# Optimization experiments

Hardware: AMD Instinct MI355X
Metric: run time of the kernel (lower is better)

The kernel has to match this reference:

```python
import jax, jax.numpy as jnp
import numpy as np

B, C, H, W_ = 4, 256, 64, 64
INTER = 128

def conv1x1(x, w, b):
    # x: [B,C,H,W], w: [O,C], b: [O] -> [B,O,H,W]
    return jnp.einsum('bchw,oc->bohw', x, w) + b[None, :, None, None]

def setup_inputs() -> dict:
    key = jax.random.key(0)
    ks = jax.random.split(key, 5)
    s_in = 1.0 / np.sqrt(C)
    s_mid = 1.0 / np.sqrt(INTER)
    return {
        'x': jax.random.normal(ks[0], (B, C, H, W_), dtype=jnp.float32),
        'w_g': jax.random.normal(ks[1], (INTER, C), dtype=jnp.float32) * s_in,
        'b_g': jnp.zeros((INTER,), dtype=jnp.float32),
        'w_theta': jax.random.normal(ks[2], (INTER, C), dtype=jnp.float32) * s_in,
        'b_theta': jnp.zeros((INTER,), dtype=jnp.float32),
        'w_phi': jax.random.normal(ks[3], (INTER, C), dtype=jnp.float32) * s_in,
        'b_phi': jnp.zeros((INTER,), dtype=jnp.float32),
        'w_out': jax.random.normal(ks[4], (C, INTER), dtype=jnp.float32) * s_mid,
        'b_out': jnp.zeros((C,), dtype=jnp.float32),
    }

def reference(x, w_g, b_g, w_theta, b_theta, w_phi, b_phi, w_out, b_out):
    b, c, h, w = x.shape
    n = h * w
    # 1x1 conv projections, flatten spatial dims to N tokens
    g_x = conv1x1(x, w_g, b_g).reshape(b, INTER, n).transpose(0, 2, 1)      # [B,N,I]
    theta_x = conv1x1(x, w_theta, b_theta).reshape(b, INTER, n).transpose(0, 2, 1)  # [B,N,I]
    phi_x = conv1x1(x, w_phi, b_phi).reshape(b, INTER, n)                   # [B,I,N]
    f = jnp.einsum('bni,bim->bnm', theta_x, phi_x)                          # [B,N,N]
    f_div_C = jax.nn.softmax(f, axis=-1)
    y = jnp.einsum('bnm,bmi->bni', f_div_C, g_x)                            # [B,N,I]
    y = y.transpose(0, 2, 1).reshape(b, INTER, h, w)
    W_y = conv1x1(y, w_out, b_out)                                          # [B,C,H,W]
    return W_y + x
```

## Files before the change

### kernel.cpp

```cpp
#include <hip/hip_runtime.h>

#define BB 4
#define CC 256
#define NN 4096
#define II 128
#define NSPLIT 4
#define KVH (NN / NSPLIT)
#define NT (KVH / 64)
#define LOG2E 1.4426950408889634f

typedef float f32x4 __attribute__((ext_vector_type(4)));
typedef _Float16 f16x8 __attribute__((ext_vector_type(8)));

static __device__ __forceinline__ unsigned short f2h(float f) {
    _Float16 h = (_Float16)f;
    return __builtin_bit_cast(unsigned short, h);
}
static __device__ __forceinline__ float h2f(unsigned short s) {
    return (float)__builtin_bit_cast(_Float16, s);
}
static __device__ __forceinline__ unsigned int pack2h(float a, float b) {
    return (unsigned int)f2h(a) | ((unsigned int)f2h(b) << 16);
}
static __device__ __forceinline__ unsigned int cvt2h(float a, float b) {
    return __builtin_bit_cast(unsigned int, __builtin_amdgcn_cvt_pkrtz(a, b));
}
#define M3(a, b, c) fmaxf(fmaxf((a), (b)), (c))

__global__ __launch_bounds__(256) void proj_kernel(
    const float* __restrict__ x,
    const float* __restrict__ w_th, const float* __restrict__ b_th,
    const float* __restrict__ w_ph, const float* __restrict__ b_ph,
    const float* __restrict__ w_g,  const float* __restrict__ b_g,
    const float* __restrict__ w_out,
    unsigned short* __restrict__ Qb, unsigned short* __restrict__ Kb,
    unsigned short* __restrict__ Vt, unsigned short* __restrict__ Wo)
{
    __shared__ char lds[24576];
    unsigned short* wl = (unsigned short*)lds;
    unsigned short* xl = (unsigned short*)(lds + 16384);

    int tid = threadIdx.x;
    int w = tid >> 6, l = tid & 63, g = l >> 4, cl = l & 15;
    int mat = blockIdx.z, b = blockIdx.y, n0 = blockIdx.x * 64;
    const float* wp = (mat == 0) ? w_th : (mat == 1) ? w_ph : w_g;
    const float* bp = (mat == 0) ? b_th : (mat == 1) ? b_ph : b_g;

    f32x4 acc[2][4];
    #pragma unroll
    for (int it = 0; it < 2; ++it)
        #pragma unroll
        for (int nt = 0; nt < 4; ++nt) acc[it][nt] = (f32x4){0.f, 0.f, 0.f, 0.f};

    const float* xb = x + (size_t)b * CC * NN;
    int c2 = tid >> 3, nch = tid & 7;

    for (int c0 = 0; c0 < CC; c0 += 64) {
        __syncthreads();
        #pragma unroll
        for (int r = 0; r < 4; ++r) {
            int idx = r * 256 + tid;
            int row = idx >> 3, ch = idx & 7;
            const float* src = wp + row * CC + c0 + ch * 8;
            float4 a = *(const float4*)src;
            float4 bq = *(const float4*)(src + 4);
            union { unsigned int u[4]; uint4 q; } pk;
            pk.u[0] = pack2h(a.x, a.y);  pk.u[1] = pack2h(a.z, a.w);
            pk.u[2] = pack2h(bq.x, bq.y); pk.u[3] = pack2h(bq.z, bq.w);
            *(uint4*)((char*)wl + row * 128 + ((ch ^ (row & 7)) << 4)) = pk.q;
        }
        {
            const float* xsrc = xb + (size_t)(c0 + c2 * 2) * NN + n0 + nch * 8;
            float4 x00 = *(const float4*)xsrc;
            float4 x01 = *(const float4*)(xsrc + 4);
            float4 x10 = *(const float4*)(xsrc + NN);
            float4 x11 = *(const float4*)(xsrc + NN + 4);
            float lo[8] = {x00.x, x00.y, x00.z, x00.w, x01.x, x01.y, x01.z, x01.w};
            float hi[8] = {x10.x, x10.y, x10.z, x10.w, x11.x, x11.y, x11.z, x11.w};
            #pragma unroll
            for (int t = 0; t < 8; ++t) {
                int n = nch * 8 + t;
                *(unsigned int*)((char*)xl + n * 128 + ((c2 * 4) ^ ((n & 7) << 4))) = pack2h(lo[t], hi[t]);
            }
        }
        __syncthreads();
        #pragma unroll
        for (int kc = 0; kc < 2; ++kc) {
            f16x8 af[2], bf[4];
            #pragma unroll
            for (int it = 0; it < 2; ++it) {
                int row = w * 32 + it * 16 + cl;
                af[it] = *(const f16x8*)((const char*)wl + row * 128 + (((kc * 4 + g) ^ (row & 7)) << 4));
            }
            #pragma unroll
            for (int nt = 0; nt < 4; ++nt) {
                int row = nt * 16 + cl;
                bf[nt] = *(const f16x8*)((const char*)xl + row * 128 + (((kc * 4 + g) ^ (row & 7)) << 4));
            }
            #pragma unroll
            for (int it = 0; it < 2; ++it)
                #pragma unroll
                for (int nt = 0; nt < 4; ++nt)
                    acc[it][nt] = __builtin_amdgcn_mfma_f32_16x16x32_f16(af[it], bf[nt], acc[it][nt], 0, 0, 0);
        }
    }

    float bv[2][4];
    #pragma unroll
    for (int it = 0; it < 2; ++it)
        #pragma unroll
        for (int r = 0; r < 4; ++r) bv[it][r] = bp[w * 32 + it * 16 + 4 * g + r];
    float scale = (mat == 0) ? LOG2E : 1.0f;

    __syncthreads();
    if (mat < 2) {
        unsigned short* pk = (unsigned short*)lds;
        #pragma unroll
        for (int it = 0; it < 2; ++it)
            #pragma unroll
            for (int nt = 0; nt < 4; ++nt)
                #pragma unroll
                for (int r = 0; r < 4; r += 2) {
                    int n = nt * 16 + cl;
                    int i = w * 32 + it * 16 + 4 * g + r;
                    unsigned int v = pack2h((acc[it][nt][r] + bv[it][r]) * scale,
                                            (acc[it][nt][r + 1] + bv[it][r + 1]) * scale);
                    *(unsigned int*)((char*)pk + n * 256 + ((i * 2) ^ ((n & 7) << 4))) = v;
                }
        __syncthreads();
        unsigned short* out = (mat == 0) ? Qb : Kb;
        #pragma unroll
        for (int r = 0; r < 4; ++r) {
            int idx = r * 256 + tid;
            int n = idx >> 4, seg = idx & 15;
            uint4 q = *(const uint4*)((const char*)pk + n * 256 + ((seg << 4) ^ ((n & 7) << 4)));
            *(uint4*)(out + (size_t)(b * NN + n0 + n) * II + seg * 8) = q;
        }
    } else {
        unsigned short* pk = (unsigned short*)lds;
        #pragma unroll
        for (int it = 0; it < 2; ++it)
            #pragma unroll
            for (int nt = 0; nt < 4; ++nt)
                #pragma unroll
                for (int r = 0; r < 4; ++r) {
                    int i = w * 32 + it * 16 + 4 * g + r;
                    int n = nt * 16 + cl;
                    *(unsigned short*)((char*)pk + i * 128 + ((n * 2) ^ ((i & 7) << 4))) =
                        f2h(acc[it][nt][r] + bv[it][r]);
                }
        __syncthreads();
        #pragma unroll
        for (int r = 0; r < 4; ++r) {
            int idx = r * 256 + tid;
            int i = idx >> 3, seg = idx & 7;
            uint4 q = *(const uint4*)((const char*)pk + i * 128 + ((seg << 4) ^ ((i & 7) << 4)));
            *(uint4*)(Vt + (size_t)(b * II + i) * NN + n0 + seg * 8) = q;
        }
        if (blockIdx.x == 0) {
            #pragma unroll
            for (int r = 0; r < 16; ++r) {
                int idx = (r * 256 + tid) * 8;
                float4 a = *(const float4*)(w_out + idx);
                float4 b4 = *(const float4*)(w_out + idx + 4);
                union { unsigned int u[4]; uint4 q; } pw;
                pw.u[0] = pack2h(a.x, a.y);   pw.u[1] = pack2h(a.z, a.w);
                pw.u[2] = pack2h(b4.x, b4.y); pw.u[3] = pack2h(b4.z, b4.w);
                *(uint4*)&Wo[idx] = pw.q;
            }
        }
    }
}

__global__ __launch_bounds__(256, 2) void attn_kernel(
    const unsigned short* __restrict__ Qb,
    const unsigned short* __restrict__ Kb,
    const unsigned short* __restrict__ Vb,
    unsigned short* __restrict__ Yp,
    float2* __restrict__ ML)
{
    __shared__ unsigned short Ks[64 * 128];
    __shared__ unsigned short Vs[128 * 64];

    int tid = threadIdx.x;
    int w = tid >> 6, l = tid & 63, g = l >> 4, cl = l & 15;
    int id = blockIdx.x;
    int comb = (id & 7) * 2 + ((id >> 3) & 1);
    int b = comb >> 2, sp = comb & 3, qt = id >> 4;
    int qr0 = qt * 128;
    int m_base = sp * KVH;

    f16x8 qa0[4], qa1[4];
    {
        const unsigned short* qrow0 = Qb + (size_t)(b * NN + qr0 + w * 32 + cl) * II;
        const unsigned short* qrow1 = qrow0 + 16 * II;
        #pragma unroll
        for (int kc = 0; kc < 4; ++kc) {
            qa0[kc] = *(const f16x8*)(qrow0 + kc * 32 + g * 8);
            qa1[kc] = *(const f16x8*)(qrow1 + kc * 32 + g * 8);
        }
    }
    const f16x8 onesv = {(_Float16)1.f, (_Float16)1.f, (_Float16)1.f, (_Float16)1.f,
                         (_Float16)1.f, (_Float16)1.f, (_Float16)1.f, (_Float16)1.f};

    f32x4 yacc0[8], yacc1[8], lacc0, lacc1;
    #pragma unroll
    for (int it = 0; it < 8; ++it) {
        yacc0[it] = (f32x4){0.f, 0.f, 0.f, 0.f};
        yacc1[it] = (f32x4){0.f, 0.f, 0.f, 0.f};
    }
    lacc0 = (f32x4){0.f, 0.f, 0.f, 0.f};
    lacc1 = (f32x4){0.f, 0.f, 0.f, 0.f};
    float mrun0 = -1e30f, mrun1 = -1e30f;

    const unsigned short* kb = Kb + (size_t)(b * NN + m_base) * II;
    const unsigned short* vb = Vb + (size_t)b * II * NN + m_base;
    int krow = tid >> 4, kch = tid & 15;
    int vrow = tid >> 3, vch = tid & 7;
    int kswz = (kch ^ (krow & 7)) << 4;
    int vsw = (vrow & 7) << 4;
    int vc0 = ((vch >> 2) * 32 + (vch & 1) * 16 + ((vch >> 1) & 1) * 4) * 2;

    uint4 k0, k1, k2, k3, v0, v1, v2, v3;
    k0 = *(const uint4*)(kb + (size_t)(krow) * II + kch * 8);
    k1 = *(const uint4*)(kb + (size_t)(16 + krow) * II + kch * 8);
    k2 = *(const uint4*)(kb + (size_t)(32 + krow) * II + kch * 8);
    k3 = *(const uint4*)(kb + (size_t)(48 + krow) * II + kch * 8);
    v0 = *(const uint4*)(vb + (size_t)(vrow) * NN + vch * 8);
    v1 = *(const uint4*)(vb + (size_t)(32 + vrow) * NN + vch * 8);
    v2 = *(const uint4*)(vb + (size_t)(64 + vrow) * NN + vch * 8);
    v3 = *(const uint4*)(vb + (size_t)(96 + vrow) * NN + vch * 8);

    for (int t = 0; t < NT; ++t) {
        __syncthreads();
        *(uint4*)((char*)Ks + (krow) * 256 + kswz) = k0;
        *(uint4*)((char*)Ks + (16 + krow) * 256 + kswz) = k1;
        *(uint4*)((char*)Ks + (32 + krow) * 256 + kswz) = k2;
        *(uint4*)((char*)Ks + (48 + krow) * 256 + kswz) = k3;
        {
            uint2 lo, hi;
            lo.x = v0.x; lo.y = v0.y; hi.x = v0.z; hi.y = v0.w;
            *(uint2*)((char*)Vs + (vrow) * 128 + (vc0 ^ vsw)) = lo;
            *(uint2*)((char*)Vs + (vrow) * 128 + ((vc0 + 16) ^ vsw)) = hi;
            lo.x = v1.x; lo.y = v1.y; hi.x = v1.z; hi.y = v1.w;
            *(uint2*)((char*)Vs + (32 + vrow) * 128 + (vc0 ^ vsw)) = lo;
            *(uint2*)((char*)Vs + (32 + vrow) * 128 + ((vc0 + 16) ^ vsw)) = hi;
            lo.x = v2.x; lo.y = v2.y; hi.x = v2.z; hi.y = v2.w;
            *(uint2*)((char*)Vs + (64 + vrow) * 128 + (vc0 ^ vsw)) = lo;
            *(uint2*)((char*)Vs + (64 + vrow) * 128 + ((vc0 + 16) ^ vsw)) = hi;
            lo.x = v3.x; lo.y = v3.y; hi.x = v3.z; hi.y = v3.w;
            *(uint2*)((char*)Vs + (96 + vrow) * 128 + (vc0 ^ vsw)) = lo;
            *(uint2*)((char*)Vs + (96 + vrow) * 128 + ((vc0 + 16) ^ vsw)) = hi;
        }
        __syncthreads();
        if (t + 1 < NT) {
            const unsigned short* kp = kb + (size_t)(t + 1) * 64 * II;
            k0 = *(const uint4*)(kp + (size_t)(krow) * II + kch * 8);
            k1 = *(const uint4*)(kp + (size_t)(16 + krow) * II + kch * 8);
            k2 = *(const uint4*)(kp + (size_t)(32 + krow) * II + kch * 8);
            k3 = *(const uint4*)(kp + (size_t)(48 + krow) * II + kch * 8);
        }

        f32x4 s0[4], s1[4];
        #pragma unroll
        for (int mt = 0; mt < 4; ++mt) {
            s0[mt] = (f32x4){0.f, 0.f, 0.f, 0.f};
            s1[mt] = (f32x4){0.f, 0.f, 0.f, 0.f};
        }
        __builtin_amdgcn_s_setprio(1);
        #pragma unroll
        for (int mt = 0; mt < 4; ++mt) {
            int row = mt * 16 + cl;
            #pragma unroll
            for (int kc = 0; kc < 4; ++kc) {
                f16x8 kf = *(const f16x8*)((const char*)Ks + row * 256 + (((kc * 4 + g) ^ (row & 7)) << 4));
                s0[mt] = __builtin_amdgcn_mfma_f32_16x16x32_f16(kf, qa0[kc], s0[mt], 0, 0, 0);
                s1[mt] = __builtin_amdgcn_mfma_f32_16x16x32_f16(kf, qa1[kc], s1[mt], 0, 0, 0);
            }
        }
        __builtin_amdgcn_s_setprio(0);
        if (t + 1 < NT) {
            const unsigned short* vp = vb + (size_t)(t + 1) * 64;
            v0 = *(const uint4*)(vp + (size_t)(vrow) * NN + vch * 8);
            v1 = *(const uint4*)(vp + (size_t)(32 + vrow) * NN + vch * 8);
            v2 = *(const uint4*)(vp + (size_t)(64 + vrow) * NN + vch * 8);
            v3 = *(const uint4*)(vp + (size_t)(96 + vrow) * NN + vch * 8);
        }

        union { unsigned int u[4]; f16x8 v; } pb00, pb01, pb10, pb11;
        {
            float t0 = M3(s0[0][0], s0[0][1], s0[0][2]);
            float t1 = M3(s0[0][3], s0[1][0], s0[1][1]);
            float t2 = M3(s0[1][2], s0[1][3], s0[2][0]);
            float t3 = M3(s0[2][1], s0[2][2], s0[2][3]);
            float t4 = M3(s0[3][0], s0[3][1], s0[3][2]);
            float tmax = fmaxf(M3(t0, t1, t2), M3(t3, t4, s0[3][3]));
            tmax = fmaxf(tmax, __shfl_xor(tmax, 16));
            tmax = fmaxf(tmax, __shfl_xor(tmax, 32));
            if (!__all(tmax <= mrun0 + 8.0f)) {
                float mnew = fmaxf(mrun0, tmax);
                float corr = exp2f(mrun0 - mnew);
                mrun0 = mnew;
                #pragma unroll
                for (int it = 0; it < 8; ++it)
                    #pragma unroll
                    for (int r = 0; r < 4; ++r) yacc0[it][r] *= corr;
                #pragma unroll
                for (int r = 0; r < 4; ++r) lacc0[r] *= corr;
            }
            #pragma unroll
            for (int mt = 0; mt < 4; ++mt) {
                unsigned int ua = cvt2h(exp2f(s0[mt][0] - mrun0), exp2f(s0[mt][1] - mrun0));
                unsigned int ub = cvt2h(exp2f(s0[mt][2] - mrun0), exp2f(s0[mt][3] - mrun0));
                if (mt < 2) { pb00.u[mt * 2] = ua; pb00.u[mt * 2 + 1] = ub; }
                else        { pb01.u[(mt - 2) * 2] = ua; pb01.u[(mt - 2) * 2 + 1] = ub; }
            }
        }
        {
            float t0 = M3(s1[0][0], s1[0][1], s1[0][2]);
            float t1 = M3(s1[0][3], s1[1][0], s1[1][1]);
            float t2 = M3(s1[1][2], s1[1][3], s1[2][0]);
            float t3 = M3(s1[2][1], s1[2][2], s1[2][3]);
            float t4 = M3(s1[3][0], s1[3][1], s1[3][2]);
            float tmax = fmaxf(M3(t0, t1, t2), M3(t3, t4, s1[3][3]));
            tmax = fmaxf(tmax, __shfl_xor(tmax, 16));
            tmax = fmaxf(tmax, __shfl_xor(tmax, 32));
            if (!__all(tmax <= mrun1 + 8.0f)) {
                float mnew = fmaxf(mrun1, tmax);
                float corr = exp2f(mrun1 - mnew);
                mrun1 = mnew;
                #pragma unroll
                for (int it = 0; it < 8; ++it)
                    #pragma unroll
                    for (int r = 0; r < 4; ++r) yacc1[it][r] *= corr;
                #pragma unroll
                for (int r = 0; r < 4; ++r) lacc1[r] *= corr;
            }
            #pragma unroll
            for (int mt = 0; mt < 4; ++mt) {
                unsigned int ua = cvt2h(exp2f(s1[mt][0] - mrun1), exp2f(s1[mt][1] - mrun1));
                unsigned int ub = cvt2h(exp2f(s1[mt][2] - mrun1), exp2f(s1[mt][3] - mrun1));
                if (mt < 2) { pb10.u[mt * 2] = ua; pb10.u[mt * 2 + 1] = ub; }
                else        { pb11.u[(mt - 2) * 2] = ua; pb11.u[(mt - 2) * 2 + 1] = ub; }
            }
        }

        __builtin_amdgcn_s_setprio(1);
        lacc0 = __builtin_amdgcn_mfma_f32_16x16x32_f16(onesv, pb00.v, lacc0, 0, 0, 0);
        lacc0 = __builtin_amdgcn_mfma_f32_16x16x32_f16(onesv, pb01.v, lacc0, 0, 0, 0);
        lacc1 = __builtin_amdgcn_mfma_f32_16x16x32_f16(onesv, pb10.v, lacc1, 0, 0, 0);
        lacc1 = __builtin_amdgcn_mfma_f32_16x16x32_f16(onesv, pb11.v, lacc1, 0, 0, 0);
        #pragma unroll
        for (int it = 0; it < 8; ++it) {
            int row = it * 16 + cl;
            f16x8 vf0 = *(const f16x8*)((const char*)Vs + row * 128 + ((g ^ (row & 7)) << 4));
            f16x8 vf1 = *(const f16x8*)((const char*)Vs + row * 128 + (((4 + g) ^ (row & 7)) << 4));
            yacc0[it] = __builtin_amdgcn_mfma_f32_16x16x32_f16(vf0, pb00.v, yacc0[it], 0, 0, 0);
            yacc0[it] = __builtin_amdgcn_mfma_f32_16x16x32_f16(vf1, pb01.v, yacc0[it], 0, 0, 0);
            yacc1[it] = __builtin_amdgcn_mfma_f32_16x16x32_f16(vf0, pb10.v, yacc1[it], 0, 0, 0);
            yacc1[it] = __builtin_amdgcn_mfma_f32_16x16x32_f16(vf1, pb11.v, yacc1[it], 0, 0, 0);
        }
        __builtin_amdgcn_s_setprio(0);
    }

    __syncthreads();

    unsigned short* ys = Ks + w * 2048;
    size_t rowbase0 = (size_t)((sp * BB + b) * NN + qr0 + w * 32);
    int prow = l >> 2;
    {
        float rl = 1.0f / lacc0[0];
        #pragma unroll
        for (int it = 0; it < 8; ++it)
            #pragma unroll
            for (int r = 0; r < 4; r += 2) {
                int i = it * 16 + 4 * g + r;
                *(unsigned int*)((char*)ys + cl * 256 + ((i * 2) ^ ((cl & 7) << 4))) =
                    pack2h(yacc0[it][r] * rl, yacc0[it][r + 1] * rl);
            }
        #pragma unroll
        for (int c = 0; c < 4; ++c) {
            int seg = c * 4 + (l & 3);
            uint4 q = *(const uint4*)((const char*)ys + prow * 256 + ((seg << 4) ^ ((prow & 7) << 4)));
            *(uint4*)(Yp + (rowbase0 + prow) * II + seg * 8) = q;
        }
    }
    {
        float rl = 1.0f / lacc1[0];
        #pragma unroll
        for (int it = 0; it < 8; ++it)
            #pragma unroll
            for (int r = 0; r < 4; r += 2) {
                int i = it * 16 + 4 * g + r;
                *(unsigned int*)((char*)ys + cl * 256 + ((i * 2) ^ ((cl & 7) << 4))) =
                    pack2h(yacc1[it][r] * rl, yacc1[it][r + 1] * rl);
            }
        #pragma unroll
        for (int c = 0; c < 4; ++c) {
            int seg = c * 4 + (l & 3);
            uint4 q = *(const uint4*)((const char*)ys + prow * 256 + ((seg << 4) ^ ((prow & 7) << 4)));
            *(uint4*)(Yp + (rowbase0 + 16 + prow) * II + seg * 8) = q;
        }
    }
    if (l < 16) {
        float2 v; v.x = mrun0; v.y = lacc0[0];
        ML[rowbase0 + l] = v;
    } else if (l < 32) {
        float2 v; v.x = mrun1; v.y = lacc1[0];
        ML[rowbase0 + 16 + (l - 16)] = v;
    }
}

__global__ __launch_bounds__(256) void combine_kernel(
    const unsigned short* __restrict__ Yp, const float2* __restrict__ ML,
    const unsigned short* __restrict__ Wo, const float* __restrict__ b_out,
    const float* __restrict__ x, float* __restrict__ out)
{
    __shared__ unsigned short Ys[4][16 * 128];

    int tid = threadIdx.x;
    int w = tid >> 6, l = tid & 63, g = l >> 4, cl = l & 15;
    int qt = blockIdx.x, b = blockIdx.y;
    int qr0 = qt * 64;
    int n = qr0 + w * 16 + cl;

    float ms[NSPLIT], ls[NSPLIT], wgt[NSPLIT];
    float M = -1e30f;
    #pragma unroll
    for (int s = 0; s < NSPLIT; ++s) {
        float2 ml = ML[(size_t)(s * BB + b) * NN + n];
        ms[s] = ml.x; ls[s] = ml.y;
        M = fmaxf(M, ml.x);
    }
    float wsum = 0.f;
    #pragma unroll
    for (int s = 0; s < NSPLIT; ++s) { wgt[s] = exp2f(ms[s] - M) * ls[s]; wsum += wgt[s]; }
    float rd = 1.0f / wsum;
    #pragma unroll
    for (int s = 0; s < NSPLIT; ++s) wgt[s] *= rd;

    unsigned short* ys = Ys[w];
    #pragma unroll
    for (int j = 0; j < 4; ++j) {
        float acc[8];
        #pragma unroll
        for (int e = 0; e < 8; ++e) acc[e] = 0.f;
        #pragma unroll
        for (int s = 0; s < NSPLIT; ++s) {
            union { unsigned short s16[8]; uint4 q; } a;
            a.q = *(const uint4*)(Yp + ((size_t)(s * BB + b) * NN + n) * II + g * 32 + j * 8);
            #pragma unroll
            for (int e = 0; e < 8; ++e) acc[e] += wgt[s] * h2f(a.s16[e]);
        }
        union { unsigned int u[4]; uint4 q; } o;
        #pragma unroll
        for (int e = 0; e < 4; ++e) o.u[e] = pack2h(acc[e * 2], acc[e * 2 + 1]);
        *(uint4*)((char*)ys + cl * 256 + (((g * 4 + j) ^ (cl & 7)) << 4)) = o.q;
    }

    f32x4 zero4 = {0.f, 0.f, 0.f, 0.f};
    f16x8 yf[4];
    #pragma unroll
    for (int kc = 0; kc < 4; ++kc)
        yf[kc] = *(const f16x8*)((const char*)ys + cl * 256 + (((kc * 4 + g) ^ (cl & 7)) << 4));
    for (int ct = 0; ct < 16; ++ct) {
        f32x4 oa = zero4;
        #pragma unroll
        for (int kc = 0; kc < 4; ++kc) {
            f16x8 wf = *(const f16x8*)(Wo + (ct * 16 + cl) * II + kc * 32 + g * 8);
            oa = __builtin_amdgcn_mfma_f32_16x16x32_f16(wf, yf[kc], oa, 0, 0, 0);
        }
        #pragma unroll
        for (int r = 0; r < 4; ++r) {
            int c = ct * 16 + 4 * g + r;
            size_t off = (size_t)(b * CC + c) * NN + n;
            out[off] = oa[r] + b_out[c] + x[off];
        }
    }
}

extern "C" void kernel_launch(void* const* d_in, const int* in_sizes, int n_in,
                              void* d_out, int out_size, void* d_ws, size_t ws_size,
                              hipStream_t stream) {
    const float* x     = (const float*)d_in[0];
    const float* w_g   = (const float*)d_in[1];
    const float* b_g   = (const float*)d_in[2];
    const float* w_th  = (const float*)d_in[3];
    const float* b_th  = (const float*)d_in[4];
    const float* w_ph  = (const float*)d_in[5];
    const float* b_ph  = (const float*)d_in[6];
    const float* w_out = (const float*)d_in[7];
    const float* b_o   = (const float*)d_in[8];
    float* out = (float*)d_out;

    const size_t SZ = (size_t)BB * NN * II;
    unsigned short* Qb = (unsigned short*)d_ws;
    unsigned short* Kb = Qb + SZ;
    unsigned short* Vt = Kb + SZ;
    unsigned short* Wo = Vt + SZ;
    unsigned short* Yp = Wo + (size_t)CC * II;
    float2*         ML = (float2*)(Yp + (size_t)NSPLIT * SZ);

    proj_kernel<<<dim3(NN / 64, BB, 3), dim3(256), 0, stream>>>(
        x, w_th, b_th, w_ph, b_ph, w_g, b_g, w_out, Qb, Kb, Vt, Wo);
    attn_kernel<<<dim3(NSPLIT * BB * (NN / 128)), dim3(256), 0, stream>>>(
        Qb, Kb, Vt, Yp, ML);
    combine_kernel<<<dim3(NN / 64, BB), dim3(256), 0, stream>>>(Yp, ML, Wo, b_o, x, out);
}
```

Measured before the change: 99.80 us.

## Fuse three projections per block and raise attention KV split to eight

The projection kernel now computes theta, phi and g in one block, staging all three weight tiles in LDS. The x tile is therefore loaded and converted once instead of three times. The attention kernel is templated on the KV split count and uses 8 splits when the workspace is large enough, with a higher occupancy hint, to give more blocks in flight. The cost is more partial outputs for the combine kernel to read and reduce, and a larger LDS footprint in the projection kernel, which lowers its occupancy.

```diff
diff --git a/kernel.cpp b/kernel.cpp
--- a/kernel.cpp
+++ b/kernel.cpp
@@ -4,9 +4,6 @@
 #define CC 256
 #define NN 4096
 #define II 128
-#define NSPLIT 4
-#define KVH (NN / NSPLIT)
-#define NT (KVH / 64)
 #define LOG2E 1.4426950408889634f
 
 typedef float f32x4 __attribute__((ext_vector_type(4)));
@@ -36,39 +33,27 @@
     unsigned short* __restrict__ Qb, unsigned short* __restrict__ Kb,
     unsigned short* __restrict__ Vt, unsigned short* __restrict__ Wo)
 {
-    __shared__ char lds[24576];
-    unsigned short* wl = (unsigned short*)lds;
-    unsigned short* xl = (unsigned short*)(lds + 16384);
+    __shared__ char lds[57344];
+    unsigned short* xl = (unsigned short*)lds;
 
     int tid = threadIdx.x;
     int w = tid >> 6, l = tid & 63, g = l >> 4, cl = l & 15;
-    int mat = blockIdx.z, b = blockIdx.y, n0 = blockIdx.x * 64;
-    const float* wp = (mat == 0) ? w_th : (mat == 1) ? w_ph : w_g;
-    const float* bp = (mat == 0) ? b_th : (mat == 1) ? b_ph : b_g;
-
-    f32x4 acc[2][4];
-    #pragma unroll
-    for (int it = 0; it < 2; ++it)
-        #pragma unroll
-        for (int nt = 0; nt < 4; ++nt) acc[it][nt] = (f32x4){0.f, 0.f, 0.f, 0.f};
+    int b = blockIdx.y, n0 = blockIdx.x * 64;
+    const float* wp0 = w_th; const float* wp1 = w_ph; const float* wp2 = w_g;
+
+    f32x4 acc[3][2][4];
+    #pragma unroll
+    for (int m = 0; m < 3; ++m)
+        #pragma unroll
+        for (int it = 0; it < 2; ++it)
+            #pragma unroll
+            for (int nt = 0; nt < 4; ++nt) acc[m][it][nt] = (f32x4){0.f, 0.f, 0.f, 0.f};
 
     const float* xb = x + (size_t)b * CC * NN;
     int c2 = tid >> 3, nch = tid & 7;
 
     for (int c0 = 0; c0 < CC; c0 += 64) {
         __syncthreads();
-        #pragma unroll
-        for (int r = 0; r < 4; ++r) {
-            int idx = r * 256 + tid;
-            int row = idx >> 3, ch = idx & 7;
-            const float* src = wp + row * CC + c0 + ch * 8;
-            float4 a = *(const float4*)src;
-            float4 bq = *(const float4*)(src + 4);
-            union { unsigned int u[4]; uint4 q; } pk;
-            pk.u[0] = pack2h(a.x, a.y);  pk.u[1] = pack2h(a.z, a.w);
-            pk.u[2] = pack2h(bq.x, bq.y); pk.u[3] = pack2h(bq.z, bq.w);
-            *(uint4*)((char*)wl + row * 128 + ((ch ^ (row & 7)) << 4)) = pk.q;
-        }
         {
             const float* xsrc = xb + (size_t)(c0 + c2 * 2) * NN + n0 + nch * 8;
             float4 x00 = *(const float4*)xsrc;
@@ -83,38 +68,59 @@
                 *(unsigned int*)((char*)xl + n * 128 + ((c2 * 4) ^ ((n & 7) << 4))) = pack2h(lo[t], hi[t]);
             }
         }
+        #pragma unroll
+        for (int r = 0; r < 12; ++r) {
+            const int mat = r >> 2;
+            int ir = (r & 3) * 32 + (tid >> 3), ch = tid & 7;
+            const float* wsrc = (mat == 0 ? wp0 : mat == 1 ? wp1 : wp2) + ir * CC + c0 + ch * 8;
+            float4 a = *(const float4*)wsrc;
+            float4 bq = *(const float4*)(wsrc + 4);
+            union { unsigned int u[4]; uint4 q; } pk;
+            pk.u[0] = pack2h(a.x, a.y);   pk.u[1] = pack2h(a.z, a.w);
+            pk.u[2] = pack2h(bq.x, bq.y); pk.u[3] = pack2h(bq.z, bq.w);
+            *(uint4*)(lds + 8192 + mat * 16384 + ir * 128 + ((ch ^ (ir & 7)) << 4)) = pk.q;
+        }
         __syncthreads();
         #pragma unroll
         for (int kc = 0; kc < 2; ++kc) {
-            f16x8 af[2], bf[4];
-            #pragma unroll
-            for (int it = 0; it < 2; ++it) {
-                int row = w * 32 + it * 16 + cl;
-                af[it] = *(const f16x8*)((const char*)wl + row * 128 + (((kc * 4 + g) ^ (row & 7)) << 4));
-            }
+            f16x8 bf[4];
             #pragma unroll
             for (int nt = 0; nt < 4; ++nt) {
                 int row = nt * 16 + cl;
                 bf[nt] = *(const f16x8*)((const char*)xl + row * 128 + (((kc * 4 + g) ^ (row & 7)) << 4));
             }
             #pragma unroll
-            for (int it = 0; it < 2; ++it)
-                #pragma unroll
-                for (int nt = 0; nt < 4; ++nt)
-                    acc[it][nt] = __builtin_amdgcn_mfma_f32_16x16x32_f16(af[it], bf[nt], acc[it][nt], 0, 0, 0);
-        }
-    }
-
-    float bv[2][4];
-    #pragma unroll
-    for (int it = 0; it < 2; ++it)
-        #pragma unroll
-        for (int r = 0; r < 4; ++r) bv[it][r] = bp[w * 32 + it * 16 + 4 * g + r];
-    float scale = (mat == 0) ? LOG2E : 1.0f;
-
-    __syncthreads();
-    if (mat < 2) {
+            for (int m = 0; m < 3; ++m) {
+                f16x8 af[2];
+                #pragma unroll
+                for (int it = 0; it < 2; ++it) {
+                    int row = w * 32 + it * 16 + cl;
+                    af[it] = *(const f16x8*)(lds + 8192 + m * 16384 + row * 128 + (((kc * 4 + g) ^ (row & 7)) << 4));
+                }
+                #pragma unroll
+                for (int it = 0; it < 2; ++it)
+                    #pragma unroll
+                    for (int nt = 0; nt < 4; ++nt)
+                        acc[m][it][nt] = __builtin_amdgcn_mfma_f32_16x16x32_f16(af[it], bf[nt], acc[m][it][nt], 0, 0, 0);
+            }
+        }
+    }
+
+    float bv[3][2][4];
+    #pragma unroll
+    for (int m = 0; m < 3; ++m) {
+        const float* bp = (m == 0) ? b_th : (m == 1) ? b_ph : b_g;
+        #pragma unroll
+        for (int it = 0; it < 2; ++it)
+            #pragma unroll
+            for (int r = 0; r < 4; ++r) bv[m][it][r] = bp[w * 32 + it * 16 + 4 * g + r];
+    }
+
+    #pragma unroll
+    for (int m = 0; m < 2; ++m) {
+        float scale = (m == 0) ? LOG2E : 1.0f;
         unsigned short* pk = (unsigned short*)lds;
+        __syncthreads();
         #pragma unroll
         for (int it = 0; it < 2; ++it)
             #pragma unroll
@@ -123,12 +129,12 @@
                 for (int r = 0; r < 4; r += 2) {
                     int n = nt * 16 + cl;
                     int i = w * 32 + it * 16 + 4 * g + r;
-                    unsigned int v = pack2h((acc[it][nt][r] + bv[it][r]) * scale,
-                                            (acc[it][nt][r + 1] + bv[it][r + 1]) * scale);
+                    unsigned int v = pack2h((acc[m][it][nt][r] + bv[m][it][r]) * scale,
+                                            (acc[m][it][nt][r + 1] + bv[m][it][r + 1]) * scale);
                     *(unsigned int*)((char*)pk + n * 256 + ((i * 2) ^ ((n & 7) << 4))) = v;
                 }
         __syncthreads();
-        unsigned short* out = (mat == 0) ? Qb : Kb;
+        unsigned short* out = (m == 0) ? Qb : Kb;
         #pragma unroll
         for (int r = 0; r < 4; ++r) {
             int idx = r * 256 + tid;
@@ -136,8 +142,10 @@
             uint4 q = *(const uint4*)((const char*)pk + n * 256 + ((seg << 4) ^ ((n & 7) << 4)));
             *(uint4*)(out + (size_t)(b * NN + n0 + n) * II + seg * 8) = q;
         }
-    } else {
+    }
+    {
         unsigned short* pk = (unsigned short*)lds;
+        __syncthreads();
         #pragma unroll
         for (int it = 0; it < 2; ++it)
             #pragma unroll
@@ -147,7 +155,7 @@
                     int i = w * 32 + it * 16 + 4 * g + r;
                     int n = nt * 16 + cl;
                     *(unsigned short*)((char*)pk + i * 128 + ((n * 2) ^ ((i & 7) << 4))) =
-                        f2h(acc[it][nt][r] + bv[it][r]);
+                        f2h(acc[2][it][nt][r] + bv[2][it][r]);
                 }
         __syncthreads();
         #pragma unroll
@@ -157,36 +165,42 @@
             uint4 q = *(const uint4*)((const char*)pk + i * 128 + ((seg << 4) ^ ((i & 7) << 4)));
             *(uint4*)(Vt + (size_t)(b * II + i) * NN + n0 + seg * 8) = q;
         }
-        if (blockIdx.x == 0) {
-            #pragma unroll
-            for (int r = 0; r < 16; ++r) {
-                int idx = (r * 256 + tid) * 8;
-                float4 a = *(const float4*)(w_out + idx);
-                float4 b4 = *(const float4*)(w_out + idx + 4);
-                union { unsigned int u[4]; uint4 q; } pw;
-                pw.u[0] = pack2h(a.x, a.y);   pw.u[1] = pack2h(a.z, a.w);
-                pw.u[2] = pack2h(b4.x, b4.y); pw.u[3] = pack2h(b4.z, b4.w);
-                *(uint4*)&Wo[idx] = pw.q;
-            }
-        }
-    }
-}
-
-__global__ __launch_bounds__(256, 2) void attn_kernel(
+    }
+    if (blockIdx.x == 0 && b == 0) {
+        #pragma unroll
+        for (int r = 0; r < 16; ++r) {
+            int idx = (r * 256 + tid) * 8;
+            float4 a = *(const float4*)(w_out + idx);
+            float4 b4 = *(const float4*)(w_out + idx + 4);
+            union { unsigned int u[4]; uint4 q; } pw;
+            pw.u[0] = pack2h(a.x, a.y);   pw.u[1] = pack2h(a.z, a.w);
+            pw.u[2] = pack2h(b4.x, b4.y); pw.u[3] = pack2h(b4.z, b4.w);
+            *(uint4*)&Wo[idx] = pw.q;
+        }
+    }
+}
+
+template<int NS>
+__global__ __launch_bounds__(256, (NS == 8) ? 4 : 2) void attn_kernel(
     const unsigned short* __restrict__ Qb,
     const unsigned short* __restrict__ Kb,
     const unsigned short* __restrict__ Vb,
     unsigned short* __restrict__ Yp,
     float2* __restrict__ ML)
 {
+    constexpr int KVH = NN / NS;
+    constexpr int NT = KVH / 64;
+    constexpr int HALF = NS / 2;
+    constexpr int QSH = (NS == 8) ? 5 : 4;
+
     __shared__ unsigned short Ks[64 * 128];
     __shared__ unsigned short Vs[128 * 64];
 
     int tid = threadIdx.x;
     int w = tid >> 6, l = tid & 63, g = l >> 4, cl = l & 15;
     int id = blockIdx.x;
-    int comb = (id & 7) * 2 + ((id >> 3) & 1);
-    int b = comb >> 2, sp = comb & 3, qt = id >> 4;
+    int comb = (id & 7) * HALF + ((id >> 3) & (HALF - 1));
+    int b = comb / NS, sp = comb % NS, qt = id >> QSH;
     int qr0 = qt * 128;
     int m_base = sp * KVH;
 
@@ -411,6 +425,7 @@
     }
 }
 
+template<int NS>
 __global__ __launch_bounds__(256) void combine_kernel(
     const unsigned short* __restrict__ Yp, const float2* __restrict__ ML,
     const unsigned short* __restrict__ Wo, const float* __restrict__ b_out,
@@ -424,20 +439,20 @@
     int qr0 = qt * 64;
     int n = qr0 + w * 16 + cl;
 
-    float ms[NSPLIT], ls[NSPLIT], wgt[NSPLIT];
+    float ms[NS], ls[NS], wgt[NS];
     float M = -1e30f;
     #pragma unroll
-    for (int s = 0; s < NSPLIT; ++s) {
+    for (int s = 0; s < NS; ++s) {
         float2 ml = ML[(size_t)(s * BB + b) * NN + n];
         ms[s] = ml.x; ls[s] = ml.y;
         M = fmaxf(M, ml.x);
     }
     float wsum = 0.f;
     #pragma unroll
-    for (int s = 0; s < NSPLIT; ++s) { wgt[s] = exp2f(ms[s] - M) * ls[s]; wsum += wgt[s]; }
+    for (int s = 0; s < NS; ++s) { wgt[s] = exp2f(ms[s] - M) * ls[s]; wsum += wgt[s]; }
     float rd = 1.0f / wsum;
     #pragma unroll
-    for (int s = 0; s < NSPLIT; ++s) wgt[s] *= rd;
+    for (int s = 0; s < NS; ++s) wgt[s] *= rd;
 
     unsigned short* ys = Ys[w];
     #pragma unroll
@@ -446,7 +461,7 @@
         #pragma unroll
         for (int e = 0; e < 8; ++e) acc[e] = 0.f;
         #pragma unroll
-        for (int s = 0; s < NSPLIT; ++s) {
+        for (int s = 0; s < NS; ++s) {
             union { unsigned short s16[8]; uint4 q; } a;
             a.q = *(const uint4*)(Yp + ((size_t)(s * BB + b) * NN + n) * II + g * 32 + j * 8);
             #pragma unroll
@@ -499,11 +514,18 @@
     unsigned short* Vt = Kb + SZ;
     unsigned short* Wo = Vt + SZ;
     unsigned short* Yp = Wo + (size_t)CC * II;
-    float2*         ML = (float2*)(Yp + (size_t)NSPLIT * SZ);
-
-    proj_kernel<<<dim3(NN / 64, BB, 3), dim3(256), 0, stream>>>(
+
+    size_t need8 = ((size_t)3 * SZ + (size_t)CC * II + (size_t)8 * SZ) * 2
+                 + (size_t)8 * BB * NN * sizeof(float2);
+    proj_kernel<<<dim3(NN / 64, BB), dim3(256), 0, stream>>>(
         x, w_th, b_th, w_ph, b_ph, w_g, b_g, w_out, Qb, Kb, Vt, Wo);
-    attn_kernel<<<dim3(NSPLIT * BB * (NN / 128)), dim3(256), 0, stream>>>(
-        Qb, Kb, Vt, Yp, ML);
-    combine_kernel<<<dim3(NN / 64, BB), dim3(256), 0, stream>>>(Yp, ML, Wo, b_o, x, out);
-}
+    if (ws_size >= need8) {
+        float2* ML = (float2*)(Yp + (size_t)8 * SZ);
+        attn_kernel<8><<<dim3(8 * BB * (NN / 128)), dim3(256), 0, stream>>>(Qb, Kb, Vt, Yp, ML);
+        combine_kernel<8><<<dim3(NN / 64, BB), dim3(256), 0, stream>>>(Yp, ML, Wo, b_o, x, out);
+    } else {
+        float2* ML = (float2*)(Yp + (size_t)4 * SZ);
+        attn_kernel<4><<<dim3(4 * BB * (NN / 128)), dim3(256), 0, stream>>>(Qb, Kb, Vt, Yp, ML);
+        combine_kernel<4><<<dim3(NN / 64, BB), dim3(256), 0, stream>>>(Yp, ML, Wo, b_o, x, out);
+    }
+}
```

Result: slower. 301.1 us (+201.7%).

## Double-buffer K/V shared tiles to drop one barrier per iteration

Applied to the files above, without the earlier changes.

Shared-memory K and V tiles become double-buffered. The next tile's global loads are issued at the start of each iteration, and their LDS stores go into the alternate buffer after QK^T and after softmax. This cuts the loop to a single __syncthreads per tile and overlaps LDS writes with MFMA work. The cost is twice the LDS footprint (64KB), which may limit occupancy at 2 blocks per CU, and all loads for the next tile are issued earlier, which raises register pressure.

```diff
diff --git a/kernel.cpp b/kernel.cpp
--- a/kernel.cpp
+++ b/kernel.cpp
@@ -179,8 +179,8 @@
     unsigned short* __restrict__ Yp,
     float2* __restrict__ ML)
 {
-    __shared__ unsigned short Ks[64 * 128];
-    __shared__ unsigned short Vs[128 * 64];
+    __shared__ unsigned short Ks[2][64 * 128];
+    __shared__ unsigned short Vs[2][128 * 64];
 
     int tid = threadIdx.x;
     int w = tid >> 6, l = tid & 63, g = l >> 4, cl = l & 15;
@@ -230,61 +230,70 @@
     v1 = *(const uint4*)(vb + (size_t)(32 + vrow) * NN + vch * 8);
     v2 = *(const uint4*)(vb + (size_t)(64 + vrow) * NN + vch * 8);
     v3 = *(const uint4*)(vb + (size_t)(96 + vrow) * NN + vch * 8);
+    {
+        *(uint4*)((char*)Ks[0] + (krow) * 256 + kswz) = k0;
+        *(uint4*)((char*)Ks[0] + (16 + krow) * 256 + kswz) = k1;
+        *(uint4*)((char*)Ks[0] + (32 + krow) * 256 + kswz) = k2;
+        *(uint4*)((char*)Ks[0] + (48 + krow) * 256 + kswz) = k3;
+        uint2 lo, hi;
+        lo.x = v0.x; lo.y = v0.y; hi.x = v0.z; hi.y = v0.w;
+        *(uint2*)((char*)Vs[0] + (vrow) * 128 + (vc0 ^ vsw)) = lo;
+        *(uint2*)((char*)Vs[0] + (vrow) * 128 + ((vc0 + 16) ^ vsw)) = hi;
+        lo.x = v1.x; lo.y = v1.y; hi.x = v1.z; hi.y = v1.w;
+        *(uint2*)((char*)Vs[0] + (32 + vrow) * 128 + (vc0 ^ vsw)) = lo;
+        *(uint2*)((char*)Vs[0] + (32 + vrow) * 128 + ((vc0 + 16) ^ vsw)) = hi;
+        lo.x = v2.x; lo.y = v2.y; hi.x = v2.z; hi.y = v2.w;
+        *(uint2*)((char*)Vs[0] + (64 + vrow) * 128 + (vc0 ^ vsw)) = lo;
+        *(uint2*)((char*)Vs[0] + (64 + vrow) * 128 + ((vc0 + 16) ^ vsw)) = hi;
+        lo.x = v3.x; lo.y = v3.y; hi.x = v3.z; hi.y = v3.w;
+        *(uint2*)((char*)Vs[0] + (96 + vrow) * 128 + (vc0 ^ vsw)) = lo;
+        *(uint2*)((char*)Vs[0] + (96 + vrow) * 128 + ((vc0 + 16) ^ vsw)) = hi;
+    }
 
     for (int t = 0; t < NT; ++t) {
         __syncthreads();
-        *(uint4*)((char*)Ks + (krow) * 256 + kswz) = k0;
-        *(uint4*)((char*)Ks + (16 + krow) * 256 + kswz) = k1;
-        *(uint4*)((char*)Ks + (32 + krow) * 256 + kswz) = k2;
-        *(uint4*)((char*)Ks + (48 + krow) * 256 + kswz) = k3;
-        {
-            uint2 lo, hi;
-            lo.x = v0.x; lo.y = v0.y; hi.x = v0.z; hi.y = v0.w;
-            *(uint2*)((char*)Vs + (vrow) * 128 + (vc0 ^ vsw)) = lo;
-            *(uint2*)((char*)Vs + (vrow) * 128 + ((vc0 + 16) ^ vsw)) = hi;
-            lo.x = v1.x; lo.y = v1.y; hi.x = v1.z; hi.y = v1.w;
-            *(uint2*)((char*)Vs + (32 + vrow) * 128 + (vc0 ^ vsw)) = lo;
-            *(uint2*)((char*)Vs + (32 + vrow) * 128 + ((vc0 + 16) ^ vsw)) = hi;
-            lo.x = v2.x; lo.y = v2.y; hi.x = v2.z; hi.y = v2.w;
-            *(uint2*)((char*)Vs + (64 + vrow) * 128 + (vc0 ^ vsw)) = lo;
-            *(uint2*)((char*)Vs + (64 + vrow) * 128 + ((vc0 + 16) ^ vsw)) = hi;
-            lo.x = v3.x; lo.y = v3.y; hi.x = v3.z; hi.y = v3.w;
-            *(uint2*)((char*)Vs + (96 + vrow) * 128 + (vc0 ^ vsw)) = lo;
-            *(uint2*)((char*)Vs + (96 + vrow) * 128 + ((vc0 + 16) ^ vsw)) = hi;
-        }
-        __syncthreads();
-        if (t + 1 < NT) {
+        const unsigned short* ksb = Ks[t & 1];
+        const unsigned short* vsb = Vs[t & 1];
+        unsigned short* kw = Ks[(t + 1) & 1];
+        unsigned short* vw = Vs[(t + 1) & 1];
+        bool more = (t + 1 < NT);
+        if (more) {
             const unsigned short* kp = kb + (size_t)(t + 1) * 64 * II;
+            const unsigned short* vp = vb + (size_t)(t + 1) * 64;
             k0 = *(const uint4*)(kp + (size_t)(krow) * II + kch * 8);
             k1 = *(const uint4*)(kp + (size_t)(16 + krow) * II + kch * 8);
             k2 = *(const uint4*)(kp + (size_t)(32 + krow) * II + kch * 8);
             k3 = *(const uint4*)(kp + (size_t)(48 + krow) * II + kch * 8);
-        }
-
-        f32x4 s0[4], s1[4];
-        #pragma unroll
-        for (int mt = 0; mt < 4; ++mt) {
-            s0[mt] = (f32x4){0.f, 0.f, 0.f, 0.f};
-            s1[mt] = (f32x4){0.f, 0.f, 0.f, 0.f};
-        }
-        __builtin_amdgcn_s_setprio(1);
-        #pragma unroll
-        for (int mt = 0; mt < 4; ++mt) {
-            int row = mt * 16 + cl;
-            #pragma unroll
-            for (int kc = 0; kc < 4; ++kc) {
-                f16x8 kf = *(const f16x8*)((const char*)Ks + row * 256 + (((kc * 4 + g) ^ (row & 7)) << 4));
-                s0[mt] = __builtin_amdgcn_mfma_f32_16x16x32_f16(kf, qa0[kc], s0[mt], 0, 0, 0);
-                s1[mt] = __builtin_amdgcn_mfma_f32_16x16x32_f16(kf, qa1[kc], s1[mt], 0, 0, 0);
-            }
-        }
-        __builtin_amdgcn_s_setprio(0);
-        if (t + 1 < NT) {
-            const unsigned short* vp = vb + (size_t)(t + 1) * 64;
             v0 = *(const uint4*)(vp + (size_t)(vrow) * NN + vch * 8);
             v1 = *(const uint4*)(vp + (size_t)(32 + vrow) * NN + vch * 8);
             v2 = *(const uint4*)(vp + (size_t)(64 + vrow) * NN + vch * 8);
             v3 = *(const uint4*)(vp + (size_t)(96 + vrow) * NN + vch * 8);
+        }
+
+        f32x4 s0[4], s1[4];
+        #pragma unroll
+        for (int mt = 0; mt < 4; ++mt) {
+            s0[mt] = (f32x4){0.f, 0.f, 0.f, 0.f};
+            s1[mt] = (f32x4){0.f, 0.f, 0.f, 0.f};
+        }
+        __builtin_amdgcn_s_setprio(1);
+        #pragma unroll
+        for (int mt = 0; mt < 4; ++mt) {
+            int row = mt * 16 + cl;
+            #pragma unroll
+            for (int kc = 0; kc < 4; ++kc) {
+                f16x8 kf = *(const f16x8*)((const char*)ksb + row * 256 + (((kc * 4 + g) ^ (row & 7)) << 4));
+                s0[mt] = __builtin_amdgcn_mfma_f32_16x16x32_f16(kf, qa0[kc], s0[mt], 0, 0, 0);
+                s1[mt] = __builtin_amdgcn_mfma_f32_16x16x32_f16(kf, qa1[kc], s1[mt], 0, 0, 0);
+            }
+        }
+        __builtin_amdgcn_s_setprio(0);
+
+        if (more) {
+            *(uint4*)((char*)kw + (krow) * 256 + kswz) = k0;
+            *(uint4*)((char*)kw + (16 + krow) * 256 + kswz) = k1;
+            *(uint4*)((char*)kw + (32 + krow) * 256 + kswz) = k2;
+            *(uint4*)((char*)kw + (48 + krow) * 256 + kswz) = k3;
         }
 
         union { unsigned int u[4]; f16x8 v; } pb00, pb01, pb10, pb11;
@@ -345,6 +354,22 @@
             }
         }
 
+        if (more) {
+            uint2 lo, hi;
+            lo.x = v0.x; lo.y = v0.y; hi.x = v0.z; hi.y = v0.w;
+            *(uint2*)((char*)vw + (vrow) * 128 + (vc0 ^ vsw)) = lo;
+            *(uint2*)((char*)vw + (vrow) * 128 + ((vc0 + 16) ^ vsw)) = hi;
+            lo.x = v1.x; lo.y = v1.y; hi.x = v1.z; hi.y = v1.w;
+            *(uint2*)((char*)vw + (32 + vrow) * 128 + (vc0 ^ vsw)) = lo;
+            *(uint2*)((char*)vw + (32 + vrow) * 128 + ((vc0 + 16) ^ vsw)) = hi;
+            lo.x = v2.x; lo.y = v2.y; hi.x = v2.z; hi.y = v2.w;
+            *(uint2*)((char*)vw + (64 + vrow) * 128 + (vc0 ^ vsw)) = lo;
+            *(uint2*)((char*)vw + (64 + vrow) * 128 + ((vc0 + 16) ^ vsw)) = hi;
+            lo.x = v3.x; lo.y = v3.y; hi.x = v3.z; hi.y = v3.w;
+            *(uint2*)((char*)vw + (96 + vrow) * 128 + (vc0 ^ vsw)) = lo;
+            *(uint2*)((char*)vw + (96 + vrow) * 128 + ((vc0 + 16) ^ vsw)) = hi;
+        }
+
         __builtin_amdgcn_s_setprio(1);
         lacc0 = __builtin_amdgcn_mfma_f32_16x16x32_f16(onesv, pb00.v, lacc0, 0, 0, 0);
         lacc0 = __builtin_amdgcn_mfma_f32_16x16x32_f16(onesv, pb01.v, lacc0, 0, 0, 0);
@@ -353,8 +378,8 @@
         #pragma unroll
         for (int it = 0; it < 8; ++it) {
             int row = it * 16 + cl;
-            f16x8 vf0 = *(const f16x8*)((const char*)Vs + row * 128 + ((g ^ (row & 7)) << 4));
-            f16x8 vf1 = *(const f16x8*)((const char*)Vs + row * 128 + (((4 + g) ^ (row & 7)) << 4));
+            f16x8 vf0 = *(const f16x8*)((const char*)vsb + row * 128 + ((g ^ (row & 7)) << 4));
+            f16x8 vf1 = *(const f16x8*)((const char*)vsb + row * 128 + (((4 + g) ^ (row & 7)) << 4));
             yacc0[it] = __builtin_amdgcn_mfma_f32_16x16x32_f16(vf0, pb00.v, yacc0[it], 0, 0, 0);
             yacc0[it] = __builtin_amdgcn_mfma_f32_16x16x32_f16(vf1, pb01.v, yacc0[it], 0, 0, 0);
             yacc1[it] = __builtin_amdgcn_mfma_f32_16x16x32_f16(vf0, pb10.v, yacc1[it], 0, 0, 0);
@@ -365,7 +390,7 @@
 
     __syncthreads();
 
-    unsigned short* ys = Ks + w * 2048;
+    unsigned short* ys = &Ks[0][w * 2048];
     size_t rowbase0 = (size_t)((sp * BB + b) * NN + qr0 + w * 32);
     int prow = l >> 2;
     {
```

New measurement: 101.0 us. Within noise of the previous version (+1.2%).
